# Performance work log

Measured on AMD Instinct MI355X. Metric: run time of the kernel, lower is better.

## Reference

```python
import jax, jax.numpy as jnp
import numpy as np

HEADS = 8
NEG_SLOPE = 0.2
N_REL = 3
N_NODES = 10000
N_EDGES = 160000
OBS = 32
ACT = 8
N_GRAPHS = 16
HC = HEADS * OBS  # 256 = heads * out_channels (dim=1)


def _rgat_layer(x, w, q, k, e, we, b, src, dst, etype, eattr):
    """PyG RGATConv, additive-self-attention, across-relation, dim=1, concat=True, eval mode."""
    N = x.shape[0]
    # relation-specific transform for every node, then per-edge gather (avoids [E,in,out] bmm)
    xw = jnp.einsum('ni,rio->nro', x, w)              # [N, R, H*C]
    outi = xw[dst, etype]                              # [E, H*C] target features
    outj = xw[src, etype]                              # [E, H*C] source features
    alpha = outi @ q + outj @ k + (eattr @ we) @ e     # [E, H]
    alpha = jax.nn.leaky_relu(alpha, NEG_SLOPE)
    # segment softmax over destination neighborhoods (PyG softmax: detached max, +1e-16)
    amax = jax.lax.stop_gradient(jax.ops.segment_max(alpha, dst, num_segments=N))
    amax = jnp.where(jnp.isfinite(amax), amax, 0.0)
    ex = jnp.exp(alpha - amax[dst])
    denom = jax.ops.segment_sum(ex, dst, num_segments=N)
    attn = ex / (denom[dst] + 1e-16)                   # [E, H]
    E_ = outj.shape[0]
    msg = attn[:, :, None] * outj.reshape(E_, HEADS, -1)  # [E, H, C]
    agg = jax.ops.segment_sum(msg, dst, num_segments=N)   # [N, H, C]
    return agg.reshape(N, -1) + b                          # concat heads + bias


def setup_inputs() -> dict:
    key = jax.random.key(0)
    ks = jax.random.split(key, 32)
    s = 0.05
    inp = {
        'x': jax.random.normal(ks[0], (N_NODES, OBS), jnp.float32),
        'edge_index': jax.random.randint(ks[1], (2, N_EDGES), 0, N_NODES),
        'edge_type': jax.random.randint(ks[2], (N_EDGES,), 0, N_REL),
        'edge_attr': jax.random.normal(ks[3], (N_EDGES, 1), jnp.float32),
        'batch': jnp.sort(jax.random.randint(ks[4], (N_NODES,), 0, N_GRAPHS)),
    }
    ins = [OBS, HC, HC]
    i = 5
    for l, cin in enumerate(ins, start=1):
        inp[f'w{l}'] = s * jax.random.normal(ks[i + 0], (N_REL, cin, HC), jnp.float32)
        inp[f'q{l}'] = s * jax.random.normal(ks[i + 1], (HC, HEADS), jnp.float32)
        inp[f'k{l}'] = s * jax.random.normal(ks[i + 2], (HC, HEADS), jnp.float32)
        inp[f'e{l}'] = s * jax.random.normal(ks[i + 3], (HC, HEADS), jnp.float32)
        inp[f'we{l}'] = s * jax.random.normal(ks[i + 4], (1, HC), jnp.float32)
        inp[f'b{l}'] = jnp.zeros((HC,), jnp.float32)
        i += 5
    inp['wlin'] = s * jax.random.normal(ks[i], (HC, ACT), jnp.float32)
    inp['blin'] = jnp.zeros((ACT,), jnp.float32)
    return inp


def reference(x, edge_index, edge_type, edge_attr, batch,
              w1, q1, k1, e1, we1, b1,
              w2, q2, k2, e2, we2, b2,
              w3, q3, k3, e3, we3, b3,
              wlin, blin):
    src, dst = edge_index[0], edge_index[1]
    h = jax.nn.relu(_rgat_layer(x, w1, q1, k1, e1, we1, b1, src, dst, edge_type, edge_attr))
    h = jax.nn.relu(_rgat_layer(h, w2, q2, k2, e2, we2, b2, src, dst, edge_type, edge_attr))
    h = jax.nn.relu(_rgat_layer(h, w3, q3, k3, e3, we3, b3, src, dst, edge_type, edge_attr))
    h = jnp.tanh(h @ wlin + blin)                        # [N, ACT]
    sums = jax.ops.segment_sum(h, batch, num_segments=N_GRAPHS)
    cnts = jax.ops.segment_sum(jnp.ones((h.shape[0], 1), h.dtype), batch, num_segments=N_GRAPHS)
    return sums / jnp.maximum(cnts, 1.0)                 # global_mean_pool -> [G, ACT]
```

## Files before the change

### kernel.cpp

```cpp
#include <hip/hip_runtime.h>
#include <math.h>

#define HEADS 8
#define HC 256
#define NREL 3
#define NEG 0.2f
#define MAXDEG 64
#define NCT 17

typedef float vfloat4 __attribute__((ext_vector_type(4)));
typedef short b16x8 __attribute__((ext_vector_type(8)));
typedef float f32x4 __attribute__((ext_vector_type(4)));
typedef unsigned short u16x8 __attribute__((ext_vector_type(8)));

__device__ __forceinline__ unsigned short f2bf(float f) {
    unsigned u = __float_as_uint(f);
    unsigned r = (u + 0x7FFFu + ((u >> 16) & 1u)) >> 16;
    return (unsigned short)r;
}
__device__ __forceinline__ float bf2f(unsigned short b) {
    return __uint_as_float(((unsigned)b) << 16);
}

__global__ void k_wprep(
    const float* __restrict__ W1, const float* __restrict__ Q1, const float* __restrict__ K1,
    const float* __restrict__ E1, const float* __restrict__ WE1,
    const float* __restrict__ W2, const float* __restrict__ Q2, const float* __restrict__ K2,
    const float* __restrict__ E2, const float* __restrict__ WE2,
    const float* __restrict__ W3, const float* __restrict__ Q3, const float* __restrict__ K3,
    const float* __restrict__ E3, const float* __restrict__ WE3,
    unsigned short* __restrict__ b1hi, unsigned short* __restrict__ b1lo,
    unsigned short* __restrict__ b2hi, unsigned short* __restrict__ b2lo,
    unsigned short* __restrict__ b3hi, unsigned short* __restrict__ b3lo,
    float* __restrict__ wee,
    const int* __restrict__ ei, const int* __restrict__ et, const float* __restrict__ ea,
    int* __restrict__ fill, int2* __restrict__ bkt,
    int nnodes, int nedges, int nwcv, int nprep) {
    int bi = blockIdx.x;
    int tid = threadIdx.x;
    if (bi < nwcv) {
        const float* w;
        unsigned short *bhi, *blo;
        int K, r, kb;
        if (bi < NREL) { w = W1; bhi = b1hi; blo = b1lo; K = 32; r = bi; kb = 0; }
        else if (bi < NREL + NREL * 8) {
            int idx = bi - NREL; w = W2; bhi = b2hi; blo = b2lo; K = HC; r = idx >> 3; kb = idx & 7;
        } else {
            int idx = bi - NREL - NREL * 8; w = W3; bhi = b3hi; blo = b3lo; K = HC; r = idx >> 3; kb = idx & 7;
        }
        int KB = K / 32;
        int ct = tid >> 4, mc = tid & 15;
        int c = ct * 16 + mc;
#pragma unroll
        for (int q = 0; q < 4; ++q) {
            u16x8 hv, lv;
#pragma unroll
            for (int j = 0; j < 8; ++j) {
                float f = w[(size_t)(r * K + kb * 32 + q * 8 + j) * HC + c];
                unsigned short h = f2bf(f);
                hv[j] = h;
                lv[j] = f2bf(f - bf2f(h));
            }
            size_t base = ((((size_t)r * NCT + ct) * KB + kb) * 64 + q * 16 + mc) * 8;
            *(u16x8*)(bhi + base) = hv;
            *(u16x8*)(blo + base) = lv;
        }
        return;
    }
    bi -= nwcv;
    if (bi >= nprep) {
        int e = (bi - nprep) * 256 + tid;
        if (e < nedges) {
            int dst = ei[nedges + e];
            int pos = atomicAdd(&fill[dst], 1);
            if (pos < MAXDEG)
                bkt[dst * MAXDEG + pos] = make_int2((ei[e] << 2) | (et[e] & 3),
                                                    __float_as_int(ea[e]));
        }
        return;
    }
    {
        int w = tid >> 5, lane = tid & 31;
        int row = bi * 8 + w;
        const float *wmat, *qm, *km, *em, *wem;
        unsigned short *bhi, *blo;
        int K, layer, lbi;
        if (row < NREL * 32) {
            layer = 0; lbi = row; K = 32;
            wmat = W1; qm = Q1; km = K1; em = E1; wem = WE1; bhi = b1hi; blo = b1lo;
        } else if (row < NREL * 32 + NREL * HC) {
            layer = 1; lbi = row - NREL * 32; K = HC;
            wmat = W2; qm = Q2; km = K2; em = E2; wem = WE2; bhi = b2hi; blo = b2lo;
        } else {
            layer = 2; lbi = row - NREL * 32 - NREL * HC; K = HC;
            wmat = W3; qm = Q3; km = K3; em = E3; wem = WE3; bhi = b3hi; blo = b3lo;
        }
        int r = lbi / K, i = lbi - r * K;
        int KB = K / 32;
        int kb = i >> 5, qq = (i >> 3) & 3, j = i & 7;
        const float* wrow = wmat + (size_t)lbi * HC;
        float pq[8] = {0.f, 0.f, 0.f, 0.f, 0.f, 0.f, 0.f, 0.f};
        float pk[8] = {0.f, 0.f, 0.f, 0.f, 0.f, 0.f, 0.f, 0.f};
#pragma unroll
        for (int it = 0; it < HC; it += 32) {
            int o = it + lane;
            float wv = wrow[o];
            float4 qa = *(const float4*)(qm + (size_t)o * 8);
            float4 qb = *(const float4*)(qm + (size_t)o * 8 + 4);
            float4 ka = *(const float4*)(km + (size_t)o * 8);
            float4 kc = *(const float4*)(km + (size_t)o * 8 + 4);
            pq[0] += wv * qa.x; pq[1] += wv * qa.y; pq[2] += wv * qa.z; pq[3] += wv * qa.w;
            pq[4] += wv * qb.x; pq[5] += wv * qb.y; pq[6] += wv * qb.z; pq[7] += wv * qb.w;
            pk[0] += wv * ka.x; pk[1] += wv * ka.y; pk[2] += wv * ka.z; pk[3] += wv * ka.w;
            pk[4] += wv * kc.x; pk[5] += wv * kc.y; pk[6] += wv * kc.z; pk[7] += wv * kc.w;
        }
#pragma unroll
        for (int off = 16; off > 0; off >>= 1) {
#pragma unroll
            for (int u = 0; u < 8; ++u) {
                pq[u] += __shfl_xor(pq[u], off, 32);
                pk[u] += __shfl_xor(pk[u], off, 32);
            }
        }
        size_t base = (((size_t)r * NCT + 16) * KB + kb) * 512 + j;
        if (lane < 16) {
            int h = lane & 7;
            bool isq = lane < 8;
            float v;
            switch (h) {
                case 0: v = isq ? pq[0] : pk[0]; break;
                case 1: v = isq ? pq[1] : pk[1]; break;
                case 2: v = isq ? pq[2] : pk[2]; break;
                case 3: v = isq ? pq[3] : pk[3]; break;
                case 4: v = isq ? pq[4] : pk[4]; break;
                case 5: v = isq ? pq[5] : pk[5]; break;
                case 6: v = isq ? pq[6] : pk[6]; break;
                default: v = isq ? pq[7] : pk[7]; break;
            }
            size_t o = base + (size_t)(qq * 16 + (isq ? 0 : 8) + h) * 8;
            unsigned short hh = f2bf(v);
            bhi[o] = hh;
            blo[o] = f2bf(v - bf2f(hh));
        }
        if (lbi == 0 && w == 0 && lane < HEADS) {
            float s = 0.f;
            for (int o = 0; o < HC; o++) s += wem[o] * em[o * HEADS + lane];
            wee[layer * HEADS + lane] = s;
        }
        return;
    }
}

template <int K, int NT, bool RAWX>
__global__ __launch_bounds__(256) void k_mfma(const unsigned short* __restrict__ pahi,
                                              const unsigned short* __restrict__ palo,
                                              const unsigned short* __restrict__ pbhi,
                                              const unsigned short* __restrict__ pblo,
                                              const float* __restrict__ xraw,
                                              float* __restrict__ xw,
                                              float* __restrict__ qdot,
                                              float* __restrict__ kdot,
                                              int nnodes, int ntiles) {
    constexpr int KB = K / 32;
    int ntg = blockIdx.x;
    int r = blockIdx.y;
    int t = threadIdx.x;
    int wv = t >> 6, lane = t & 63;
    int q = lane >> 4, m = lane & 15;
    f32x4 acc[5][NT] = {};
    for (int kb = 0; kb < KB; ++kb) {
        b16x8 ah[NT], al[NT];
#pragma unroll
        for (int ti = 0; ti < NT; ++ti) {
            int nt = ntg * NT + ti;
            if (nt >= ntiles) nt = ntiles - 1;
            if constexpr (RAWX) {
                int row = nt * 16 + m;
                if (row >= nnodes) row = nnodes - 1;
                const float4* xr = (const float4*)(xraw + (size_t)row * 32 + q * 8);
                float4 f0 = xr[0], f1 = xr[1];
                float fv[8] = {f0.x, f0.y, f0.z, f0.w, f1.x, f1.y, f1.z, f1.w};
#pragma unroll
                for (int j = 0; j < 8; ++j) {
                    unsigned short hh = f2bf(fv[j]);
                    ah[ti][j] = (short)hh;
                    al[ti][j] = (short)f2bf(fv[j] - bf2f(hh));
                }
            } else {
                size_t ao = (((size_t)nt * KB + kb) * 64 + lane) * 8;
                ah[ti] = *(const b16x8*)(pahi + ao);
                al[ti] = *(const b16x8*)(palo + ao);
            }
        }
#pragma unroll
        for (int s = 0; s < 5; ++s) {
            int ct = wv + 4 * s;
            if (ct >= NCT) continue;
            size_t o = (((size_t)r * NCT + ct) * KB + kb) * 512 + (size_t)lane * 8;
            b16x8 vbh = *(const b16x8*)(pbhi + o);
            b16x8 vbl = *(const b16x8*)(pblo + o);
#pragma unroll
            for (int ti = 0; ti < NT; ++ti) {
                acc[s][ti] = __builtin_amdgcn_mfma_f32_16x16x32_bf16(ah[ti], vbh, acc[s][ti], 0, 0, 0);
                acc[s][ti] = __builtin_amdgcn_mfma_f32_16x16x32_bf16(al[ti], vbh, acc[s][ti], 0, 0, 0);
                acc[s][ti] = __builtin_amdgcn_mfma_f32_16x16x32_bf16(ah[ti], vbl, acc[s][ti], 0, 0, 0);
            }
        }
    }
#pragma unroll
    for (int ti = 0; ti < NT; ++ti) {
        int nt = ntg * NT + ti;
        if (nt >= ntiles) continue;
        int n0 = nt * 16;
#pragma unroll
        for (int s = 0; s < 5; ++s) {
            int ct = wv + 4 * s;
            if (ct >= NCT) continue;
            if (ct < 16) {
                int c = ct * 16 + m;
#pragma unroll
                for (int g = 0; g < 4; ++g) {
                    int n = n0 + q * 4 + g;
                    if (n < nnodes) xw[((size_t)n * NREL + r) * HC + c] = acc[s][ti][g];
                }
            } else {
#pragma unroll
                for (int g = 0; g < 4; ++g) {
                    int n = n0 + q * 4 + g;
                    if (n < nnodes) {
                        if (m < 8) qdot[n * 24 + r * 8 + m] = acc[s][ti][g];
                        else       kdot[n * 24 + r * 8 + (m - 8)] = acc[s][ti][g];
                    }
                }
            }
        }
    }
}

__global__ __launch_bounds__(256) void k_agg(const float* __restrict__ xw,
                      const float* __restrict__ qdot, const float* __restrict__ kdot,
                      const int* __restrict__ fill, const int2* __restrict__ bkt,
                      const float* __restrict__ wee,
                      const float* __restrict__ bias,
                      unsigned short* __restrict__ houthi, unsigned short* __restrict__ houtlo,
                      float* __restrict__ out8,
                      const float* __restrict__ wlin, const float* __restrict__ blin,
                      int nnodes) {
    __shared__ float salpha[4][MAXDEG * HEADS];
    __shared__ int spack[4][MAXDEG];
    int wv = threadIdx.x >> 6, lane = threadIdx.x & 63;
    int n = blockIdx.x * 4 + wv;
    if (n >= nnodes) return;
    int beg = n * MAXDEG;
    int deg = fill[n];
    if (deg > MAXDEG) deg = MAXDEG;
    float* sal = salpha[wv];
    int* spk = spack[wv];
    if (lane < deg) {
        int2 pa = bkt[beg + lane];
        int pk = pa.x;
        float ae = __int_as_float(pa.y);
        int s = pk >> 2, t = pk & 3;
        spk[lane] = pk;
        float4 q0 = *(const float4*)(qdot + n * 24 + t * 8);
        float4 q1 = *(const float4*)(qdot + n * 24 + t * 8 + 4);
        float4 k0 = *(const float4*)(kdot + s * 24 + t * 8);
        float4 k1 = *(const float4*)(kdot + s * 24 + t * 8 + 4);
        float4 w0 = *(const float4*)(wee);
        float4 w1 = *(const float4*)(wee + 4);
        float a0 = q0.x + k0.x + ae * w0.x;
        float a1 = q0.y + k0.y + ae * w0.y;
        float a2 = q0.z + k0.z + ae * w0.z;
        float a3 = q0.w + k0.w + ae * w0.w;
        float a4 = q1.x + k1.x + ae * w1.x;
        float a5 = q1.y + k1.y + ae * w1.y;
        float a6 = q1.z + k1.z + ae * w1.z;
        float a7 = q1.w + k1.w + ae * w1.w;
        a0 = (a0 > 0.f) ? a0 : NEG * a0;
        a1 = (a1 > 0.f) ? a1 : NEG * a1;
        a2 = (a2 > 0.f) ? a2 : NEG * a2;
        a3 = (a3 > 0.f) ? a3 : NEG * a3;
        a4 = (a4 > 0.f) ? a4 : NEG * a4;
        a5 = (a5 > 0.f) ? a5 : NEG * a5;
        a6 = (a6 > 0.f) ? a6 : NEG * a6;
        a7 = (a7 > 0.f) ? a7 : NEG * a7;
        *(float4*)(sal + lane * 8) = make_float4(a0, a1, a2, a3);
        *(float4*)(sal + lane * 8 + 4) = make_float4(a4, a5, a6, a7);
    }
#define ROWP(pkv) ((const float4*)(xw + ((size_t)((pkv) >> 2) * NREL + ((pkv) & 3)) * HC))
    float4 vA[8], vB[8];
    int nb8 = deg >> 3;
    if (nb8 >= 1) {
#pragma unroll
        for (int u = 0; u < 8; ++u) vA[u] = ROWP(spk[u])[lane];
    }
    float sinv_h;
    {
        int h = lane & 7, c = lane >> 3;
        float m = -INFINITY;
        for (int d = c; d < deg; d += 8) m = fmaxf(m, sal[d * 8 + h]);
        m = fmaxf(m, __shfl_xor(m, 8, 64));
        m = fmaxf(m, __shfl_xor(m, 16, 64));
        m = fmaxf(m, __shfl_xor(m, 32, 64));
        float s = 0.f;
        for (int d = c; d < deg; d += 8) {
            float ex = expf(sal[d * 8 + h] - m);
            sal[d * 8 + h] = ex;
            s += ex;
        }
        s += __shfl_xor(s, 8, 64);
        s += __shfl_xor(s, 16, 64);
        s += __shfl_xor(s, 32, 64);
        sinv_h = 1.f / (s + 1e-16f);
    }
    float sinv_sel = __shfl(sinv_h, lane >> 3, 64);
    int hsel = lane >> 3;
    float4 acc4 = make_float4(0.f, 0.f, 0.f, 0.f);
    int d = 0;
#define CONS(buf, base)                                                        \
    {                                                                          \
        _Pragma("unroll") for (int u = 0; u < 8; ++u) {                        \
            float av = sal[((base) + u) * 8 + hsel];                           \
            acc4.x += av * buf[u].x;                                           \
            acc4.y += av * buf[u].y;                                           \
            acc4.z += av * buf[u].z;                                           \
            acc4.w += av * buf[u].w;                                           \
        }                                                                      \
    }
    if (nb8 >= 1) {
        for (;;) {
            int dn = d + 8;
            if (dn + 8 <= deg) {
#pragma unroll
                for (int u = 0; u < 8; ++u) vB[u] = ROWP(spk[dn + u])[lane];
                CONS(vA, d);
                d = dn;
                int dn2 = d + 8;
                if (dn2 + 8 <= deg) {
#pragma unroll
                    for (int u = 0; u < 8; ++u) vA[u] = ROWP(spk[dn2 + u])[lane];
                    CONS(vB, d);
                    d = dn2;
                } else {
                    CONS(vB, d);
                    d = dn2;
                    break;
                }
            } else {
                CONS(vA, d);
                d = dn;
                break;
            }
        }
    }
    for (; d + 3 < deg; d += 4) {
        int pk0 = spk[d], pk1 = spk[d + 1], pk2 = spk[d + 2], pk3 = spk[d + 3];
        const float4* r0 = ROWP(pk0);
        const float4* r1 = ROWP(pk1);
        const float4* r2 = ROWP(pk2);
        const float4* r3 = ROWP(pk3);
        float4 v0 = r0[lane], v1 = r1[lane], v2 = r2[lane], v3 = r3[lane];
        float a0 = sal[d * 8 + hsel];
        float a1 = sal[(d + 1) * 8 + hsel];
        float a2 = sal[(d + 2) * 8 + hsel];
        float a3 = sal[(d + 3) * 8 + hsel];
        acc4.x += a0 * v0.x + a1 * v1.x + a2 * v2.x + a3 * v3.x;
        acc4.y += a0 * v0.y + a1 * v1.y + a2 * v2.y + a3 * v3.y;
        acc4.z += a0 * v0.z + a1 * v1.z + a2 * v2.z + a3 * v3.z;
        acc4.w += a0 * v0.w + a1 * v1.w + a2 * v2.w + a3 * v3.w;
    }
    for (; d < deg; ++d) {
        int pk = spk[d];
        const float4* r0 = ROWP(pk);
        float4 v0 = r0[lane];
        float a0 = sal[d * 8 + hsel];
        acc4.x += a0 * v0.x;
        acc4.y += a0 * v0.y;
        acc4.z += a0 * v0.z;
        acc4.w += a0 * v0.w;
    }
#undef CONS
#undef ROWP
    float4 bv = *(const float4*)(bias + lane * 4);
    float vv4[4];
    vv4[0] = fmaxf(acc4.x * sinv_sel + bv.x, 0.f);
    vv4[1] = fmaxf(acc4.y * sinv_sel + bv.y, 0.f);
    vv4[2] = fmaxf(acc4.z * sinv_sel + bv.z, 0.f);
    vv4[3] = fmaxf(acc4.w * sinv_sel + bv.w, 0.f);
    if (houthi) {
        int ntile = n >> 4, mm = n & 15;
#pragma unroll
        for (int i = 0; i < 4; ++i) {
            int c = lane * 4 + i;
            int kb = c >> 5, q = (c >> 3) & 3, j = c & 7;
            size_t o2 = ((((size_t)ntile * 8 + kb) * 64) + q * 16 + mm) * 8 + j;
            unsigned short hh = f2bf(vv4[i]);
            houthi[o2] = hh;
            houtlo[o2] = f2bf(vv4[i] - bf2f(hh));
        }
    }
    if (out8) {
        float part[8] = {0.f, 0.f, 0.f, 0.f, 0.f, 0.f, 0.f, 0.f};
#pragma unroll
        for (int i = 0; i < 4; ++i) {
            const float4* wr = (const float4*)(wlin + (size_t)(lane * 4 + i) * 8);
            float4 wa = wr[0], wb = wr[1];
            float vi = vv4[i];
            part[0] += vi * wa.x; part[1] += vi * wa.y;
            part[2] += vi * wa.z; part[3] += vi * wa.w;
            part[4] += vi * wb.x; part[5] += vi * wb.y;
            part[6] += vi * wb.z; part[7] += vi * wb.w;
        }
#pragma unroll
        for (int off = 32; off > 0; off >>= 1) {
#pragma unroll
            for (int u = 0; u < 8; ++u) part[u] += __shfl_xor(part[u], off, 64);
        }
        if (lane < 8) {
            float sel;
            switch (lane) {
                case 0: sel = part[0]; break;
                case 1: sel = part[1]; break;
                case 2: sel = part[2]; break;
                case 3: sel = part[3]; break;
                case 4: sel = part[4]; break;
                case 5: sel = part[5]; break;
                case 6: sel = part[6]; break;
                default: sel = part[7]; break;
            }
            out8[(size_t)n * 8 + lane] = tanhf(sel + blin[lane]);
        }
    }
}

__global__ __launch_bounds__(256) void k_pool8(const float* __restrict__ out8,
                                               const int* __restrict__ batch,
                                               float* __restrict__ out, int nnodes) {
    int g = blockIdx.x;
    __shared__ int sb[2];
    __shared__ float sred[256];
    if (threadIdx.x < 2) {
        int target = g + threadIdx.x;
        int lo = 0, hi = nnodes;
        while (lo < hi) { int mid = (lo + hi) >> 1; if (batch[mid] < target) lo = mid + 1; else hi = mid; }
        sb[threadIdx.x] = lo;
    }
    __syncthreads();
    int beg = sb[0], end = sb[1];
    int t = threadIdx.x, h = t & 7, c = t >> 3;
    float s0 = 0.f, s1 = 0.f, s2 = 0.f, s3 = 0.f;
    int i = beg + c;
    for (; i + 96 < end; i += 128) {
        s0 += out8[(size_t)i * 8 + h];
        s1 += out8[(size_t)(i + 32) * 8 + h];
        s2 += out8[(size_t)(i + 64) * 8 + h];
        s3 += out8[(size_t)(i + 96) * 8 + h];
    }
    for (; i < end; i += 32) s0 += out8[(size_t)i * 8 + h];
    sred[t] = (s0 + s1) + (s2 + s3);
    __syncthreads();
    if (t < 8) {
        float a = 0.f;
        for (int j = 0; j < 32; ++j) a += sred[t + 8 * j];
        out[g * 8 + t] = a / fmaxf((float)(end - beg), 1.f);
    }
}


extern "C" void kernel_launch(void* const* d_in, const int* in_sizes, int n_in,
                              void* d_out, int out_size, void* d_ws, size_t ws_size,
                              hipStream_t stream) {
    const float* x    = (const float*)d_in[0];
    const int*   ei   = (const int*)d_in[1];
    const int*   et   = (const int*)d_in[2];
    const float* ea   = (const float*)d_in[3];
    const int*   batch = (const int*)d_in[4];
    const float* W[3]  = {(const float*)d_in[5],  (const float*)d_in[11], (const float*)d_in[17]};
    const float* Q[3]  = {(const float*)d_in[6],  (const float*)d_in[12], (const float*)d_in[18]};
    const float* K[3]  = {(const float*)d_in[7],  (const float*)d_in[13], (const float*)d_in[19]};
    const float* Em[3] = {(const float*)d_in[8],  (const float*)d_in[14], (const float*)d_in[20]};
    const float* WE[3] = {(const float*)d_in[9],  (const float*)d_in[15], (const float*)d_in[21]};
    const float* B[3]  = {(const float*)d_in[10], (const float*)d_in[16], (const float*)d_in[22]};
    const float* wlin = (const float*)d_in[23];
    const float* blin = (const float*)d_in[24];

    int nnodes = in_sizes[0] / 32;
    int nedges = in_sizes[2];
    int ngraph = 16;
    int npad = (nnodes + 15) & ~15;
    int ntiles = npad / 16;

    char* ws = (char*)d_ws;
    size_t off = 0;
    auto alloc = [&](size_t bytes) -> void* {
        void* p = ws + off;
        off = (off + bytes + 255) & ~(size_t)255;
        return p;
    };
    int*   fill     = (int*)alloc((size_t)(nnodes + 64) * 4);
    int2*  bkt      = (int2*)alloc((size_t)nnodes * MAXDEG * 8);
    float* xw       = (float*)alloc((size_t)npad * NREL * HC * 4);
    float* qdot     = (float*)alloc((size_t)npad * NREL * HEADS * 4);
    float* kdot     = (float*)alloc((size_t)npad * NREL * HEADS * 4);
    float* wee      = (float*)alloc((size_t)NREL * HEADS * 4);
    float* out8     = (float*)alloc((size_t)npad * 8 * 4);
    unsigned short* hahi = (unsigned short*)alloc((size_t)npad * HC * 2);
    unsigned short* halo = (unsigned short*)alloc((size_t)npad * HC * 2);
    unsigned short* hbhi = (unsigned short*)alloc((size_t)npad * HC * 2);
    unsigned short* hblo = (unsigned short*)alloc((size_t)npad * HC * 2);
    unsigned short* wt1hi = (unsigned short*)alloc((size_t)NREL * NCT * 1 * 512 * 2);
    unsigned short* wt1lo = (unsigned short*)alloc((size_t)NREL * NCT * 1 * 512 * 2);
    unsigned short* wt2hi = (unsigned short*)alloc((size_t)NREL * NCT * 8 * 512 * 2);
    unsigned short* wt2lo = (unsigned short*)alloc((size_t)NREL * NCT * 8 * 512 * 2);
    unsigned short* wt3hi = (unsigned short*)alloc((size_t)NREL * NCT * 8 * 512 * 2);
    unsigned short* wt3lo = (unsigned short*)alloc((size_t)NREL * NCT * 8 * 512 * 2);
    (void)ws_size; (void)n_in; (void)out_size;

    int nwcv = NREL * (1 + 8 + 8);
    int nprep = (NREL * 32 + 2 * NREL * HC) / 8;
    int nscat = (nedges + 255) / 256;

    hipMemsetAsync(fill, 0, (size_t)(nnodes + 64) * 4, stream);
    k_wprep<<<nwcv + nprep + nscat, 256, 0, stream>>>(
        W[0], Q[0], K[0], Em[0], WE[0],
        W[1], Q[1], K[1], Em[1], WE[1],
        W[2], Q[2], K[2], Em[2], WE[2],
        wt1hi, wt1lo, wt2hi, wt2lo, wt3hi, wt3lo, wee,
        ei, et, ea, fill, bkt,
        nnodes, nedges, nwcv, nprep);

    dim3 gmfma((ntiles + 1) / 2, NREL);
    int gagg = (nnodes + 3) / 4;

    k_mfma<32, 2, true><<<gmfma, 256, 0, stream>>>(nullptr, nullptr, wt1hi, wt1lo, x,
                                                   xw, qdot, kdot, nnodes, ntiles);
    k_agg<<<gagg, 256, 0, stream>>>(xw, qdot, kdot, fill, bkt, wee + 0, B[0],
                                    hahi, halo, nullptr, nullptr, nullptr, nnodes);

    k_mfma<HC, 2, false><<<gmfma, 256, 0, stream>>>(hahi, halo, wt2hi, wt2lo, nullptr,
                                                    xw, qdot, kdot, nnodes, ntiles);
    k_agg<<<gagg, 256, 0, stream>>>(xw, qdot, kdot, fill, bkt, wee + 8, B[1],
                                    hbhi, hblo, nullptr, nullptr, nullptr, nnodes);

    k_mfma<HC, 2, false><<<gmfma, 256, 0, stream>>>(hbhi, hblo, wt3hi, wt3lo, nullptr,
                                                    xw, qdot, kdot, nnodes, ntiles);
    k_agg<<<gagg, 256, 0, stream>>>(xw, qdot, kdot, fill, bkt, wee + 16, B[2],
                                    nullptr, nullptr, out8, wlin, blin, nnodes);

    k_pool8<<<ngraph, 256, 0, stream>>>(out8, batch, (float*)d_out, nnodes);
}
```

Measured before the change: 292.5 us.

## Fuse layer-1 MFMA with layer-2/3 weight prep and widen node tiles

Layer-2 and layer-3 weight conversion and q/k projection folding move out of the initial prep kernel into a new combined kernel that also runs the layer-1 MFMA transform. The prep kernel keeps only layer-1 weight work and the edge bucketing, so the layer-1 transform launches after less dependent work and the later weights are prepared in parallel with it. Layers 2 and 3 now use four node tiles per block instead of two, giving more A/B reuse per B-fragment load but more accumulator registers per thread, which could lower occupancy. The wee computation guard changes slightly, since lbi==0 now fires per row instead of only in warp 0.

```diff
diff --git a/kernel.cpp b/kernel.cpp
--- a/kernel.cpp
+++ b/kernel.cpp
@@ -8,7 +8,6 @@
 #define MAXDEG 64
 #define NCT 17
 
-typedef float vfloat4 __attribute__((ext_vector_type(4)));
 typedef short b16x8 __attribute__((ext_vector_type(8)));
 typedef float f32x4 __attribute__((ext_vector_type(4)));
 typedef unsigned short u16x8 __attribute__((ext_vector_type(8)));
@@ -20,6 +19,201 @@
 }
 __device__ __forceinline__ float bf2f(unsigned short b) {
     return __uint_as_float(((unsigned)b) << 16);
+}
+
+
+__device__ __forceinline__ void wconv_block(
+    int wbi,
+    const float* __restrict__ W1, const float* __restrict__ W2, const float* __restrict__ W3,
+    unsigned short* __restrict__ b1hi, unsigned short* __restrict__ b1lo,
+    unsigned short* __restrict__ b2hi, unsigned short* __restrict__ b2lo,
+    unsigned short* __restrict__ b3hi, unsigned short* __restrict__ b3lo, int tid) {
+    const float* w;
+    unsigned short *bhi, *blo;
+    int K, r, kb;
+    if (wbi < NREL) { w = W1; bhi = b1hi; blo = b1lo; K = 32; r = wbi; kb = 0; }
+    else if (wbi < NREL + NREL * 8) {
+        int idx = wbi - NREL; w = W2; bhi = b2hi; blo = b2lo; K = HC; r = idx >> 3; kb = idx & 7;
+    } else {
+        int idx = wbi - NREL - NREL * 8; w = W3; bhi = b3hi; blo = b3lo; K = HC; r = idx >> 3; kb = idx & 7;
+    }
+    int KB = K / 32;
+    int ct = tid >> 4, mc = tid & 15;
+    int c = ct * 16 + mc;
+#pragma unroll
+    for (int q = 0; q < 4; ++q) {
+        u16x8 hv, lv;
+#pragma unroll
+        for (int j = 0; j < 8; ++j) {
+            float f = w[(size_t)(r * K + kb * 32 + q * 8 + j) * HC + c];
+            unsigned short h = f2bf(f);
+            hv[j] = h;
+            lv[j] = f2bf(f - bf2f(h));
+        }
+        size_t base = ((((size_t)r * NCT + ct) * KB + kb) * 64 + q * 16 + mc) * 8;
+        *(u16x8*)(bhi + base) = hv;
+        *(u16x8*)(blo + base) = lv;
+    }
+}
+
+__device__ __forceinline__ void qkdot_warp(
+    int row, int lane,
+    const float* __restrict__ W1, const float* __restrict__ Q1, const float* __restrict__ K1,
+    const float* __restrict__ E1, const float* __restrict__ WE1,
+    const float* __restrict__ W2, const float* __restrict__ Q2, const float* __restrict__ K2,
+    const float* __restrict__ E2, const float* __restrict__ WE2,
+    const float* __restrict__ W3, const float* __restrict__ Q3, const float* __restrict__ K3,
+    const float* __restrict__ E3, const float* __restrict__ WE3,
+    unsigned short* __restrict__ b1hi, unsigned short* __restrict__ b1lo,
+    unsigned short* __restrict__ b2hi, unsigned short* __restrict__ b2lo,
+    unsigned short* __restrict__ b3hi, unsigned short* __restrict__ b3lo,
+    float* __restrict__ wee) {
+    const float *wmat, *qm, *km, *em, *wem;
+    unsigned short *bhi, *blo;
+    int K, layer, lbi;
+    if (row < NREL * 32) {
+        layer = 0; lbi = row; K = 32;
+        wmat = W1; qm = Q1; km = K1; em = E1; wem = WE1; bhi = b1hi; blo = b1lo;
+    } else if (row < NREL * 32 + NREL * HC) {
+        layer = 1; lbi = row - NREL * 32; K = HC;
+        wmat = W2; qm = Q2; km = K2; em = E2; wem = WE2; bhi = b2hi; blo = b2lo;
+    } else {
+        layer = 2; lbi = row - NREL * 32 - NREL * HC; K = HC;
+        wmat = W3; qm = Q3; km = K3; em = E3; wem = WE3; bhi = b3hi; blo = b3lo;
+    }
+    int r = lbi / K, i = lbi - r * K;
+    int KB = K / 32;
+    int kb = i >> 5, qq = (i >> 3) & 3, j = i & 7;
+    const float* wrow = wmat + (size_t)lbi * HC;
+    float pq[8] = {0.f, 0.f, 0.f, 0.f, 0.f, 0.f, 0.f, 0.f};
+    float pk[8] = {0.f, 0.f, 0.f, 0.f, 0.f, 0.f, 0.f, 0.f};
+#pragma unroll
+    for (int it = 0; it < HC; it += 32) {
+        int o = it + lane;
+        float wv = wrow[o];
+        float4 qa = *(const float4*)(qm + (size_t)o * 8);
+        float4 qb = *(const float4*)(qm + (size_t)o * 8 + 4);
+        float4 ka = *(const float4*)(km + (size_t)o * 8);
+        float4 kc = *(const float4*)(km + (size_t)o * 8 + 4);
+        pq[0] += wv * qa.x; pq[1] += wv * qa.y; pq[2] += wv * qa.z; pq[3] += wv * qa.w;
+        pq[4] += wv * qb.x; pq[5] += wv * qb.y; pq[6] += wv * qb.z; pq[7] += wv * qb.w;
+        pk[0] += wv * ka.x; pk[1] += wv * ka.y; pk[2] += wv * ka.z; pk[3] += wv * ka.w;
+        pk[4] += wv * kc.x; pk[5] += wv * kc.y; pk[6] += wv * kc.z; pk[7] += wv * kc.w;
+    }
+#pragma unroll
+    for (int off = 16; off > 0; off >>= 1) {
+#pragma unroll
+        for (int u = 0; u < 8; ++u) {
+            pq[u] += __shfl_xor(pq[u], off, 32);
+            pk[u] += __shfl_xor(pk[u], off, 32);
+        }
+    }
+    size_t base = (((size_t)r * NCT + 16) * KB + kb) * 512 + j;
+    if (lane < 16) {
+        int h = lane & 7;
+        bool isq = lane < 8;
+        float v;
+        switch (h) {
+            case 0: v = isq ? pq[0] : pk[0]; break;
+            case 1: v = isq ? pq[1] : pk[1]; break;
+            case 2: v = isq ? pq[2] : pk[2]; break;
+            case 3: v = isq ? pq[3] : pk[3]; break;
+            case 4: v = isq ? pq[4] : pk[4]; break;
+            case 5: v = isq ? pq[5] : pk[5]; break;
+            case 6: v = isq ? pq[6] : pk[6]; break;
+            default: v = isq ? pq[7] : pk[7]; break;
+        }
+        size_t o = base + (size_t)(qq * 16 + (isq ? 0 : 8) + h) * 8;
+        unsigned short hh = f2bf(v);
+        bhi[o] = hh;
+        blo[o] = f2bf(v - bf2f(hh));
+    }
+    if (lbi == 0 && lane < HEADS) {
+        float s = 0.f;
+        for (int o = 0; o < HC; o++) s += wem[o] * em[o * HEADS + lane];
+        wee[layer * HEADS + lane] = s;
+    }
+}
+
+template <int K, int NT, bool RAWX>
+__device__ __forceinline__ void mfma_block(
+    int ntg, int r,
+    const unsigned short* __restrict__ pahi, const unsigned short* __restrict__ palo,
+    const unsigned short* __restrict__ pbhi, const unsigned short* __restrict__ pblo,
+    const float* __restrict__ xraw,
+    float* __restrict__ xw, float* __restrict__ qdot, float* __restrict__ kdot,
+    int nnodes, int ntiles, int t) {
+    constexpr int KB = K / 32;
+    int wv = t >> 6, lane = t & 63;
+    int q = lane >> 4, m = lane & 15;
+    f32x4 acc[5][NT] = {};
+    for (int kb = 0; kb < KB; ++kb) {
+        b16x8 ah[NT], al[NT];
+#pragma unroll
+        for (int ti = 0; ti < NT; ++ti) {
+            int nt = ntg * NT + ti;
+            if (nt >= ntiles) nt = ntiles - 1;
+            if constexpr (RAWX) {
+                int row = nt * 16 + m;
+                if (row >= nnodes) row = nnodes - 1;
+                const float4* xr = (const float4*)(xraw + (size_t)row * 32 + q * 8);
+                float4 f0 = xr[0], f1 = xr[1];
+                float fv[8] = {f0.x, f0.y, f0.z, f0.w, f1.x, f1.y, f1.z, f1.w};
+#pragma unroll
+                for (int j = 0; j < 8; ++j) {
+                    unsigned short hh = f2bf(fv[j]);
+                    ah[ti][j] = (short)hh;
+                    al[ti][j] = (short)f2bf(fv[j] - bf2f(hh));
+                }
+            } else {
+                size_t ao = (((size_t)nt * KB + kb) * 64 + lane) * 8;
+                ah[ti] = *(const b16x8*)(pahi + ao);
+                al[ti] = *(const b16x8*)(palo + ao);
+            }
+        }
+#pragma unroll
+        for (int s = 0; s < 5; ++s) {
+            int ct = wv + 4 * s;
+            if (ct >= NCT) continue;
+            size_t o = (((size_t)r * NCT + ct) * KB + kb) * 512 + (size_t)lane * 8;
+            b16x8 vbh = *(const b16x8*)(pbhi + o);
+            b16x8 vbl = *(const b16x8*)(pblo + o);
+#pragma unroll
+            for (int ti = 0; ti < NT; ++ti) {
+                acc[s][ti] = __builtin_amdgcn_mfma_f32_16x16x32_bf16(ah[ti], vbh, acc[s][ti], 0, 0, 0);
+                acc[s][ti] = __builtin_amdgcn_mfma_f32_16x16x32_bf16(al[ti], vbh, acc[s][ti], 0, 0, 0);
+                acc[s][ti] = __builtin_amdgcn_mfma_f32_16x16x32_bf16(ah[ti], vbl, acc[s][ti], 0, 0, 0);
+            }
+        }
+    }
+#pragma unroll
+    for (int ti = 0; ti < NT; ++ti) {
+        int nt = ntg * NT + ti;
+        if (nt >= ntiles) continue;
+        int n0 = nt * 16;
+#pragma unroll
+        for (int s = 0; s < 5; ++s) {
+            int ct = wv + 4 * s;
+            if (ct >= NCT) continue;
+            if (ct < 16) {
+                int c = ct * 16 + m;
+#pragma unroll
+                for (int g = 0; g < 4; ++g) {
+                    int n = n0 + q * 4 + g;
+                    if (n < nnodes) xw[((size_t)n * NREL + r) * HC + c] = acc[s][ti][g];
+                }
+            } else {
+#pragma unroll
+                for (int g = 0; g < 4; ++g) {
+                    int n = n0 + q * 4 + g;
+                    if (n < nnodes) {
+                        if (m < 8) qdot[n * 24 + r * 8 + m] = acc[s][ti][g];
+                        else       kdot[n * 24 + r * 8 + (m - 8)] = acc[s][ti][g];
+                    }
+                }
+            }
+        }
+    }
 }
 
 __global__ void k_wprep(
@@ -39,32 +233,7 @@
     int bi = blockIdx.x;
     int tid = threadIdx.x;
     if (bi < nwcv) {
-        const float* w;
-        unsigned short *bhi, *blo;
-        int K, r, kb;
-        if (bi < NREL) { w = W1; bhi = b1hi; blo = b1lo; K = 32; r = bi; kb = 0; }
-        else if (bi < NREL + NREL * 8) {
-            int idx = bi - NREL; w = W2; bhi = b2hi; blo = b2lo; K = HC; r = idx >> 3; kb = idx & 7;
-        } else {
-            int idx = bi - NREL - NREL * 8; w = W3; bhi = b3hi; blo = b3lo; K = HC; r = idx >> 3; kb = idx & 7;
-        }
-        int KB = K / 32;
-        int ct = tid >> 4, mc = tid & 15;
-        int c = ct * 16 + mc;
-#pragma unroll
-        for (int q = 0; q < 4; ++q) {
-            u16x8 hv, lv;
-#pragma unroll
-            for (int j = 0; j < 8; ++j) {
-                float f = w[(size_t)(r * K + kb * 32 + q * 8 + j) * HC + c];
-                unsigned short h = f2bf(f);
-                hv[j] = h;
-                lv[j] = f2bf(f - bf2f(h));
-            }
-            size_t base = ((((size_t)r * NCT + ct) * KB + kb) * 64 + q * 16 + mc) * 8;
-            *(u16x8*)(bhi + base) = hv;
-            *(u16x8*)(blo + base) = lv;
-        }
+        wconv_block(bi, W1, W2, W3, b1hi, b1lo, b2hi, b2lo, b3hi, b3lo, tid);
         return;
     }
     bi -= nwcv;
@@ -79,162 +248,56 @@
         }
         return;
     }
-    {
-        int w = tid >> 5, lane = tid & 31;
-        int row = bi * 8 + w;
-        const float *wmat, *qm, *km, *em, *wem;
-        unsigned short *bhi, *blo;
-        int K, layer, lbi;
-        if (row < NREL * 32) {
-            layer = 0; lbi = row; K = 32;
-            wmat = W1; qm = Q1; km = K1; em = E1; wem = WE1; bhi = b1hi; blo = b1lo;
-        } else if (row < NREL * 32 + NREL * HC) {
-            layer = 1; lbi = row - NREL * 32; K = HC;
-            wmat = W2; qm = Q2; km = K2; em = E2; wem = WE2; bhi = b2hi; blo = b2lo;
-        } else {
-            layer = 2; lbi = row - NREL * 32 - NREL * HC; K = HC;
-            wmat = W3; qm = Q3; km = K3; em = E3; wem = WE3; bhi = b3hi; blo = b3lo;
-        }
-        int r = lbi / K, i = lbi - r * K;
-        int KB = K / 32;
-        int kb = i >> 5, qq = (i >> 3) & 3, j = i & 7;
-        const float* wrow = wmat + (size_t)lbi * HC;
-        float pq[8] = {0.f, 0.f, 0.f, 0.f, 0.f, 0.f, 0.f, 0.f};
-        float pk[8] = {0.f, 0.f, 0.f, 0.f, 0.f, 0.f, 0.f, 0.f};
-#pragma unroll
-        for (int it = 0; it < HC; it += 32) {
-            int o = it + lane;
-            float wv = wrow[o];
-            float4 qa = *(const float4*)(qm + (size_t)o * 8);
-            float4 qb = *(const float4*)(qm + (size_t)o * 8 + 4);
-            float4 ka = *(const float4*)(km + (size_t)o * 8);
-            float4 kc = *(const float4*)(km + (size_t)o * 8 + 4);
-            pq[0] += wv * qa.x; pq[1] += wv * qa.y; pq[2] += wv * qa.z; pq[3] += wv * qa.w;
-            pq[4] += wv * qb.x; pq[5] += wv * qb.y; pq[6] += wv * qb.z; pq[7] += wv * qb.w;
-            pk[0] += wv * ka.x; pk[1] += wv * ka.y; pk[2] += wv * ka.z; pk[3] += wv * ka.w;
-            pk[4] += wv * kc.x; pk[5] += wv * kc.y; pk[6] += wv * kc.z; pk[7] += wv * kc.w;
-        }
-#pragma unroll
-        for (int off = 16; off > 0; off >>= 1) {
-#pragma unroll
-            for (int u = 0; u < 8; ++u) {
-                pq[u] += __shfl_xor(pq[u], off, 32);
-                pk[u] += __shfl_xor(pk[u], off, 32);
-            }
-        }
-        size_t base = (((size_t)r * NCT + 16) * KB + kb) * 512 + j;
-        if (lane < 16) {
-            int h = lane & 7;
-            bool isq = lane < 8;
-            float v;
-            switch (h) {
-                case 0: v = isq ? pq[0] : pk[0]; break;
-                case 1: v = isq ? pq[1] : pk[1]; break;
-                case 2: v = isq ? pq[2] : pk[2]; break;
-                case 3: v = isq ? pq[3] : pk[3]; break;
-                case 4: v = isq ? pq[4] : pk[4]; break;
-                case 5: v = isq ? pq[5] : pk[5]; break;
-                case 6: v = isq ? pq[6] : pk[6]; break;
-                default: v = isq ? pq[7] : pk[7]; break;
-            }
-            size_t o = base + (size_t)(qq * 16 + (isq ? 0 : 8) + h) * 8;
-            unsigned short hh = f2bf(v);
-            bhi[o] = hh;
-            blo[o] = f2bf(v - bf2f(hh));
-        }
-        if (lbi == 0 && w == 0 && lane < HEADS) {
-            float s = 0.f;
-            for (int o = 0; o < HC; o++) s += wem[o] * em[o * HEADS + lane];
-            wee[layer * HEADS + lane] = s;
-        }
+    qkdot_warp(bi * 8 + (tid >> 5), tid & 31,
+               W1, Q1, K1, E1, WE1, W2, Q2, K2, E2, WE2, W3, Q3, K3, E3, WE3,
+               b1hi, b1lo, b2hi, b2lo, b3hi, b3lo, wee);
+}
+
+__global__ __launch_bounds__(256) void k_mfprep(
+    const float* __restrict__ W1, const float* __restrict__ Q1, const float* __restrict__ K1,
+    const float* __restrict__ E1, const float* __restrict__ WE1,
+    const float* __restrict__ W2, const float* __restrict__ Q2, const float* __restrict__ K2,
+    const float* __restrict__ E2, const float* __restrict__ WE2,
+    const float* __restrict__ W3, const float* __restrict__ Q3, const float* __restrict__ K3,
+    const float* __restrict__ E3, const float* __restrict__ WE3,
+    unsigned short* __restrict__ b1hi, unsigned short* __restrict__ b1lo,
+    unsigned short* __restrict__ b2hi, unsigned short* __restrict__ b2lo,
+    unsigned short* __restrict__ b3hi, unsigned short* __restrict__ b3lo,
+    float* __restrict__ wee,
+    const float* __restrict__ xraw,
+    float* __restrict__ xw, float* __restrict__ qdot, float* __restrict__ kdot,
+    int nnodes, int ntiles) {
+    int bi = blockIdx.x;
+    int tid = threadIdx.x;
+    int ngx = (ntiles + 1) / 2;
+    int nmf = ngx * NREL;
+    if (bi < nmf) {
+        mfma_block<32, 2, true>(bi % ngx, bi / ngx, nullptr, nullptr, b1hi, b1lo,
+                                xraw, xw, qdot, kdot, nnodes, ntiles, tid);
         return;
     }
-}
-
-template <int K, int NT, bool RAWX>
+    bi -= nmf;
+    if (bi < 48) {
+        wconv_block(NREL + bi, W1, W2, W3, b1hi, b1lo, b2hi, b2lo, b3hi, b3lo, tid);
+        return;
+    }
+    bi -= 48;
+    qkdot_warp(NREL * 32 + bi * 8 + (tid >> 5), tid & 31,
+               W1, Q1, K1, E1, WE1, W2, Q2, K2, E2, WE2, W3, Q3, K3, E3, WE3,
+               b1hi, b1lo, b2hi, b2lo, b3hi, b3lo, wee);
+}
+
+template <int K, int NT>
 __global__ __launch_bounds__(256) void k_mfma(const unsigned short* __restrict__ pahi,
                                               const unsigned short* __restrict__ palo,
                                               const unsigned short* __restrict__ pbhi,
                                               const unsigned short* __restrict__ pblo,
-                                              const float* __restrict__ xraw,
                                               float* __restrict__ xw,
                                               float* __restrict__ qdot,
                                               float* __restrict__ kdot,
                                               int nnodes, int ntiles) {
-    constexpr int KB = K / 32;
-    int ntg = blockIdx.x;
-    int r = blockIdx.y;
-    int t = threadIdx.x;
-    int wv = t >> 6, lane = t & 63;
-    int q = lane >> 4, m = lane & 15;
-    f32x4 acc[5][NT] = {};
-    for (int kb = 0; kb < KB; ++kb) {
-        b16x8 ah[NT], al[NT];
-#pragma unroll
-        for (int ti = 0; ti < NT; ++ti) {
-            int nt = ntg * NT + ti;
-            if (nt >= ntiles) nt = ntiles - 1;
-            if constexpr (RAWX) {
-                int row = nt * 16 + m;
-                if (row >= nnodes) row = nnodes - 1;
-                const float4* xr = (const float4*)(xraw + (size_t)row * 32 + q * 8);
-                float4 f0 = xr[0], f1 = xr[1];
-                float fv[8] = {f0.x, f0.y, f0.z, f0.w, f1.x, f1.y, f1.z, f1.w};
-#pragma unroll
-                for (int j = 0; j < 8; ++j) {
-                    unsigned short hh = f2bf(fv[j]);
-                    ah[ti][j] = (short)hh;
-                    al[ti][j] = (short)f2bf(fv[j] - bf2f(hh));
-                }
-            } else {
-                size_t ao = (((size_t)nt * KB + kb) * 64 + lane) * 8;
-                ah[ti] = *(const b16x8*)(pahi + ao);
-                al[ti] = *(const b16x8*)(palo + ao);
-            }
-        }
-#pragma unroll
-        for (int s = 0; s < 5; ++s) {
-            int ct = wv + 4 * s;
-            if (ct >= NCT) continue;
-            size_t o = (((size_t)r * NCT + ct) * KB + kb) * 512 + (size_t)lane * 8;
-            b16x8 vbh = *(const b16x8*)(pbhi + o);
-            b16x8 vbl = *(const b16x8*)(pblo + o);
-#pragma unroll
-            for (int ti = 0; ti < NT; ++ti) {
-                acc[s][ti] = __builtin_amdgcn_mfma_f32_16x16x32_bf16(ah[ti], vbh, acc[s][ti], 0, 0, 0);
-                acc[s][ti] = __builtin_amdgcn_mfma_f32_16x16x32_bf16(al[ti], vbh, acc[s][ti], 0, 0, 0);
-                acc[s][ti] = __builtin_amdgcn_mfma_f32_16x16x32_bf16(ah[ti], vbl, acc[s][ti], 0, 0, 0);
-            }
-        }
-    }
-#pragma unroll
-    for (int ti = 0; ti < NT; ++ti) {
-        int nt = ntg * NT + ti;
-        if (nt >= ntiles) continue;
-        int n0 = nt * 16;
-#pragma unroll
-        for (int s = 0; s < 5; ++s) {
-            int ct = wv + 4 * s;
-            if (ct >= NCT) continue;
-            if (ct < 16) {
-                int c = ct * 16 + m;
-#pragma unroll
-                for (int g = 0; g < 4; ++g) {
-                    int n = n0 + q * 4 + g;
-                    if (n < nnodes) xw[((size_t)n * NREL + r) * HC + c] = acc[s][ti][g];
-                }
-            } else {
-#pragma unroll
-                for (int g = 0; g < 4; ++g) {
-                    int n = n0 + q * 4 + g;
-                    if (n < nnodes) {
-                        if (m < 8) qdot[n * 24 + r * 8 + m] = acc[s][ti][g];
-                        else       kdot[n * 24 + r * 8 + (m - 8)] = acc[s][ti][g];
-                    }
-                }
-            }
-        }
-    }
+    mfma_block<K, NT, false>(blockIdx.x, blockIdx.y, pahi, palo, pbhi, pblo, nullptr,
+                             xw, qdot, kdot, nnodes, ntiles, threadIdx.x);
 }
 
 __global__ __launch_bounds__(256) void k_agg(const float* __restrict__ xw,
@@ -516,34 +579,37 @@
     unsigned short* wt3lo = (unsigned short*)alloc((size_t)NREL * NCT * 8 * 512 * 2);
     (void)ws_size; (void)n_in; (void)out_size;
 
-    int nwcv = NREL * (1 + 8 + 8);
-    int nprep = (NREL * 32 + 2 * NREL * HC) / 8;
     int nscat = (nedges + 255) / 256;
 
     hipMemsetAsync(fill, 0, (size_t)(nnodes + 64) * 4, stream);
-    k_wprep<<<nwcv + nprep + nscat, 256, 0, stream>>>(
+    k_wprep<<<3 + 12 + nscat, 256, 0, stream>>>(
         W[0], Q[0], K[0], Em[0], WE[0],
         W[1], Q[1], K[1], Em[1], WE[1],
         W[2], Q[2], K[2], Em[2], WE[2],
         wt1hi, wt1lo, wt2hi, wt2lo, wt3hi, wt3lo, wee,
         ei, et, ea, fill, bkt,
-        nnodes, nedges, nwcv, nprep);
-
-    dim3 gmfma((ntiles + 1) / 2, NREL);
+        nnodes, nedges, 3, 12);
+
     int gagg = (nnodes + 3) / 4;
-
-    k_mfma<32, 2, true><<<gmfma, 256, 0, stream>>>(nullptr, nullptr, wt1hi, wt1lo, x,
-                                                   xw, qdot, kdot, nnodes, ntiles);
+    int ngx2 = (ntiles + 1) / 2;
+
+    k_mfprep<<<ngx2 * NREL + 48 + 192, 256, 0, stream>>>(
+        W[0], Q[0], K[0], Em[0], WE[0],
+        W[1], Q[1], K[1], Em[1], WE[1],
+        W[2], Q[2], K[2], Em[2], WE[2],
+        wt1hi, wt1lo, wt2hi, wt2lo, wt3hi, wt3lo, wee,
+        x, xw, qdot, kdot, nnodes, ntiles);
     k_agg<<<gagg, 256, 0, stream>>>(xw, qdot, kdot, fill, bkt, wee + 0, B[0],
                                     hahi, halo, nullptr, nullptr, nullptr, nnodes);
 
-    k_mfma<HC, 2, false><<<gmfma, 256, 0, stream>>>(hahi, halo, wt2hi, wt2lo, nullptr,
-                                                    xw, qdot, kdot, nnodes, ntiles);
+    dim3 g4((ntiles + 3) / 4, NREL);
+    k_mfma<HC, 4><<<g4, 256, 0, stream>>>(hahi, halo, wt2hi, wt2lo,
+                                          xw, qdot, kdot, nnodes, ntiles);
     k_agg<<<gagg, 256, 0, stream>>>(xw, qdot, kdot, fill, bkt, wee + 8, B[1],
                                     hbhi, hblo, nullptr, nullptr, nullptr, nnodes);
 
-    k_mfma<HC, 2, false><<<gmfma, 256, 0, stream>>>(hbhi, hblo, wt3hi, wt3lo, nullptr,
-                                                    xw, qdot, kdot, nnodes, ntiles);
+    k_mfma<HC, 4><<<g4, 256, 0, stream>>>(hbhi, hblo, wt3hi, wt3lo,
+                                          xw, qdot, kdot, nnodes, ntiles);
     k_agg<<<gagg, 256, 0, stream>>>(xw, qdot, kdot, fill, bkt, wee + 16, B[2],
                                     nullptr, nullptr, out8, wlin, blin, nnodes);
 
```

Result: slower. 301.3 us (+3.0%).
